# Kernel optimization log

Measured on AMD Instinct MI355X. Metric: run time of the kernel, lower is better.

The kernel has to match this reference:

```python
import jax, jax.numpy as jnp
import numpy as np

B, S, H, NH = 2, 2048, 1024, 16
HD = H // NH  # 64
BASE = 10000.0


def _rope_tables(seq_len, head_dim):
    inv_freq = 1.0 / (BASE ** (jnp.arange(0, head_dim, 2, dtype=jnp.float32) / head_dim))
    t = jnp.arange(seq_len, dtype=jnp.float32)
    freqs = jnp.outer(t, inv_freq)            # [S, HD/2]
    emb = jnp.concatenate([freqs, freqs], -1)  # [S, HD]
    return jnp.cos(emb), jnp.sin(emb)


def _rotate_half(x):
    x1, x2 = jnp.split(x, 2, axis=-1)
    return jnp.concatenate([-x2, x1], axis=-1)


def setup_inputs() -> dict:
    key = jax.random.key(0)
    ks = jax.random.split(key, 5)
    sc = 1.0 / np.sqrt(H)
    return {
        "hidden_states": jax.random.normal(ks[0], (B, S, H), jnp.float32),
        "Wq": jax.random.normal(ks[1], (H, H), jnp.float32) * sc,
        "Wk": jax.random.normal(ks[2], (H, H), jnp.float32) * sc,
        "Wv": jax.random.normal(ks[3], (H, H), jnp.float32) * sc,
        "Wo": jax.random.normal(ks[4], (H, H), jnp.float32) * sc,
    }


def reference(hidden_states, Wq, Wk, Wv, Wo):
    b, s, h = hidden_states.shape
    # nn.Linear: y = x @ W.T
    q = hidden_states @ Wq.T
    k = hidden_states @ Wk.T
    v = hidden_states @ Wv.T
    # [B, NH, S, HD]
    q = q.reshape(b, s, NH, HD).transpose(0, 2, 1, 3)
    k = k.reshape(b, s, NH, HD).transpose(0, 2, 1, 3)
    v = v.reshape(b, s, NH, HD).transpose(0, 2, 1, 3)
    cos, sin = _rope_tables(s, HD)  # [S, HD], broadcast over B, NH
    q = q * cos + _rotate_half(q) * sin
    k = k * cos + _rotate_half(k) * sin
    scores = jnp.einsum('bhqd,bhkd->bhqk', q, k) / jnp.sqrt(jnp.float32(HD))
    probs = jax.nn.softmax(scores, axis=-1)
    ctx = jnp.einsum('bhqk,bhkd->bhqd', probs, v)
    ctx = ctx.transpose(0, 2, 1, 3).reshape(b, s, h)
    return ctx @ Wo.T
```

## Files before the change

### kernel.cpp

```cpp
#include <hip/hip_runtime.h>
#include <hip/hip_bf16.h>
#include <math.h>

typedef __hip_bfloat16 bf16;
typedef float f32x4 __attribute__((ext_vector_type(4)));
typedef float f32x16 __attribute__((ext_vector_type(16)));
typedef short s16x8 __attribute__((ext_vector_type(8)));

#define NB 2
#define SEQ 2048
#define HID 1024
#define NHEAD 16
#define HD 64
#define BH (NB * NHEAD)
#define MROWS (NB * SEQ)
#define QSCL 0.18033688011111793f

static __device__ __forceinline__ f32x4 mfma16(s16x8 a, s16x8 b, f32x4 c) {
  return __builtin_amdgcn_mfma_f32_16x16x32_bf16(a, b, c, 0, 0, 0);
}
static __device__ __forceinline__ f32x16 mfma32(s16x8 a, s16x8 b, f32x16 c) {
  return __builtin_amdgcn_mfma_f32_32x32x16_bf16(a, b, c, 0, 0, 0);
}

static __device__ __forceinline__ void gload_lds16(const bf16* g, bf16* l) {
  __builtin_amdgcn_global_load_lds((const __attribute__((address_space(1))) void*)g,
                                   (__attribute__((address_space(3))) void*)l, 16, 0, 0);
}

static __device__ __forceinline__ unsigned pack_bf16(float a, float b) {
  __hip_bfloat162 t = __float22bfloat162_rn(float2{a, b});
  return *(unsigned*)&t;
}

__global__ __launch_bounds__(256) void prep_kernel(const float* __restrict__ X,
                                                   const float* __restrict__ wq, const float* __restrict__ wk,
                                                   const float* __restrict__ wv, const float* __restrict__ wo,
                                                   bf16* __restrict__ Xb, bf16* __restrict__ wqkv,
                                                   bf16* __restrict__ wob,
                                                   float* __restrict__ ct, float* __restrict__ st) {
  int bid = blockIdx.x, tid = threadIdx.x;
  if (bid < 8192) {
    const float* src;
    bf16* dst;
    int i;
    if (bid < 4096) {
      src = X; dst = Xb;
      i = (bid * 256 + tid) * 4;
    } else {
      int wsel = (bid - 4096) >> 10;
      src = (wsel == 0) ? wq : (wsel == 1) ? wk : (wsel == 2) ? wv : wo;
      dst = (wsel < 3) ? (wqkv + (size_t)wsel * HID * HID) : wob;
      i = (((bid - 4096) & 1023) * 256 + tid) * 4;
    }
    float4 v = *(const float4*)(src + i);
    bf16 a0 = __float2bfloat16(v.x), a1 = __float2bfloat16(v.y);
    bf16 a2 = __float2bfloat16(v.z), a3 = __float2bfloat16(v.w);
    ushort4 u;
    u.x = *(const unsigned short*)&a0;
    u.y = *(const unsigned short*)&a1;
    u.z = *(const unsigned short*)&a2;
    u.w = *(const unsigned short*)&a3;
    *(ushort4*)(dst + i) = u;
  } else {
    int i = (bid - 8192) * 256 + tid;
    int s = i >> 5, j = i & 31;
    float inv = expf(-(float)(2 * j) * (9.210340371976184f / 64.0f));
    float ang = (float)s * inv;
    float sn, cs;
    sincosf(ang, &sn, &cs);
    ct[i] = cs;
    st[i] = sn;
  }
}

template <int MODE>
__global__ __launch_bounds__(256) void gemm_bt(const bf16* __restrict__ A, const bf16* __restrict__ Bm,
                                               float* __restrict__ C,
                                               bf16* __restrict__ Qb, bf16* __restrict__ Kb,
                                               bf16* __restrict__ Vtg,
                                               const float* __restrict__ ct, const float* __restrict__ st,
                                               int M, int N, int K) {
  __shared__ __align__(16) bf16 As[128][32];
  __shared__ __align__(16) bf16 Bs[128][32];
  const int tid = threadIdx.x, lane = tid & 63, wid = tid >> 6;
  const int wm = wid >> 1, wn = wid & 1;
  const int tm = blockIdx.y * 128, tn = blockIdx.x * 128;
  const int lrow = lane >> 2;
  const int lcol = (lane & 3) * 8;

  f32x4 acc[4][4];
#pragma unroll
  for (int i = 0; i < 4; ++i)
#pragma unroll
    for (int j = 0; j < 4; ++j) acc[i][j] = (f32x4){0.f, 0.f, 0.f, 0.f};

  for (int k0 = 0; k0 < K; k0 += 32) {
    __syncthreads();
    {
      int r0 = wid * 32;
      gload_lds16(A  + (size_t)(tm + r0 +      lrow) * K + k0 + lcol, &As[r0][0]);
      gload_lds16(A  + (size_t)(tm + r0 + 16 + lrow) * K + k0 + lcol, &As[r0 + 16][0]);
      gload_lds16(Bm + (size_t)(tn + r0 +      lrow) * K + k0 + lcol, &Bs[r0][0]);
      gload_lds16(Bm + (size_t)(tn + r0 + 16 + lrow) * K + k0 + lcol, &Bs[r0 + 16][0]);
    }
    __syncthreads();
    s16x8 af[4], bfr[4];
#pragma unroll
    for (int mi = 0; mi < 4; ++mi)
      af[mi] = *(const s16x8*)&As[wm * 64 + mi * 16 + (lane & 15)][(lane >> 4) * 8];
#pragma unroll
    for (int ni = 0; ni < 4; ++ni)
      bfr[ni] = *(const s16x8*)&Bs[wn * 64 + ni * 16 + (lane & 15)][(lane >> 4) * 8];
#pragma unroll
    for (int mi = 0; mi < 4; ++mi)
#pragma unroll
      for (int ni = 0; ni < 4; ++ni)
        acc[mi][ni] = mfma16(af[mi], bfr[ni], acc[mi][ni]);
  }

  if (MODE == 0) {
    const int tblk = tn >> 10;
    if (tblk < 2) {
      const float scl = (tblk == 0) ? QSCL : 1.0f;
#pragma unroll
      for (int mi = 0; mi < 4; ++mi) {
#pragma unroll
        for (int r = 0; r < 4; ++r) {
          int row = tm + wm * 64 + mi * 16 + (lane >> 4) * 4 + r;
          int s = row & (SEQ - 1);
#pragma unroll
          for (int p = 0; p < 2; ++p) {
            int j = p * 16 + (lane & 15);
            float c = ct[s * 32 + j], sn = st[s * 32 + j];
            float x0 = acc[mi][p][r], x1 = acc[mi][p + 2][r];
            acc[mi][p][r]     = (x0 * c - x1 * sn) * scl;
            acc[mi][p + 2][r] = (x1 * c + x0 * sn) * scl;
          }
        }
      }
    }
  }

#pragma unroll
  for (int mi = 0; mi < 4; ++mi) {
#pragma unroll
    for (int ni = 0; ni < 4; ++ni) {
#pragma unroll
      for (int r = 0; r < 4; ++r) {
        int row = tm + wm * 64 + mi * 16 + (lane >> 4) * 4 + r;
        int col = tn + wn * 64 + ni * 16 + (lane & 15);
        float v = acc[mi][ni][r];
        if (MODE == 0) {
          int t = col >> 10, c = col & (HID - 1);
          int h = c >> 6, d = c & 63;
          int b = row >> 11, s = row & (SEQ - 1);
          size_t bh = (size_t)(b * NHEAD + h);
          if (t == 0)      Qb[(bh * SEQ + s) * HD + d]  = __float2bfloat16(v);
          else if (t == 1) Kb[(bh * SEQ + s) * HD + d]  = __float2bfloat16(v);
          else             Vtg[(bh * HD + d) * SEQ + s] = __float2bfloat16(v);
        } else {
          C[(size_t)row * N + col] = v;
        }
      }
    }
  }
}

__global__ __launch_bounds__(512, 4) void attn_kernel(const bf16* __restrict__ Q, const bf16* __restrict__ K,
                                                      const bf16* __restrict__ Vt, bf16* __restrict__ ctx) {
  __shared__ __align__(16) bf16 S[32768];
  const int tid = threadIdx.x, l = tid & 63, w = tid >> 6;
  const int lq = l & 31, hi = l >> 5;
  const int grp = w >> 2, wq = w & 3;
  const int gtid = tid & 255;

  const int id = blockIdx.x;
  const int lin = (id & 7) * 64 + (id >> 3);
  const int bh = lin >> 4, qb = lin & 15;

  const bf16* Qp  = Q  + ((size_t)bh * SEQ + qb * 128) * HD;
  const bf16* Kp0 = K  + (size_t)bh * SEQ * HD;
  const bf16* Vp0 = Vt + (size_t)bh * HD * SEQ;

  bf16* Ksg = S + grp * 16384;
  bf16* Vsg = S + grp * 16384 + 8192;

  s16x8 qf[4];
  {
    const bf16* qr = Qp + (wq * 32 + lq) * HD + hi * 8;
#pragma unroll
    for (int ks = 0; ks < 4; ++ks) qf[ks] = *(const s16x8*)(qr + ks * 16);
  }

  s16x8 onesf;
  {
    union { unsigned u[4]; s16x8 v; } oo;
#pragma unroll
    for (int j = 0; j < 4; ++j) oo.u[j] = 0x3F803F80u;
    onesf = oo.v;
  }

  const int s0 = gtid, s1 = gtid + 256;
  const int R0 = s0 >> 3, R1 = s1 >> 3;
  const int c0 = (((s0 & 7) ^ (R0 & 7) ^ ((R0 >> 3) & 3))) * 8;
  const int c1 = (((s1 & 7) ^ (R1 & 7) ^ ((R1 >> 3) & 3))) * 8;
  const int p0 = (R0 & 51) | ((R0 & 4) << 1) | ((R0 & 8) >> 1);
  const int p1 = (R1 & 51) | ((R1 & 4) << 1) | ((R1 & 8) >> 1);
  const bf16* kS0 = Kp0 + p0 * HD + c0;
  const bf16* kS1 = Kp0 + p1 * HD + c1;
  const bf16* vS0 = Vp0 + (size_t)R0 * SEQ + c0;
  const bf16* vS1 = Vp0 + (size_t)R1 * SEQ + c1;

#define STAGE(t, b)                                                        \
  do {                                                                     \
    gload_lds16(kS0 + (size_t)(t) * (64 * HD), Ksg + (b) * 4096 + s0 * 8); \
    gload_lds16(kS1 + (size_t)(t) * (64 * HD), Ksg + (b) * 4096 + s1 * 8); \
    gload_lds16(vS0 + (t) * 64,                Vsg + (b) * 4096 + s0 * 8); \
    gload_lds16(vS1 + (t) * 64,                Vsg + (b) * 4096 + s1 * 8); \
  } while (0)

  const int base = grp * 16;
  STAGE(base + 0, 0);

  f32x16 acc0{}, acc1{};
  f32x16 lones{};

  const int rsx = (lq & 7) ^ ((lq >> 3) & 3);

  const int NSTEP = 16;
  for (int t = 0; t < NSTEP; ++t) {
    const int cur = t & 1;
    __builtin_amdgcn_s_barrier();
    if (t + 1 < NSTEP) {
      STAGE(base + t + 1, cur ^ 1);
      asm volatile("s_waitcnt vmcnt(4)" ::: "memory");
    } else {
      asm volatile("s_waitcnt vmcnt(0)" ::: "memory");
    }
    __builtin_amdgcn_sched_barrier(0);
    __builtin_amdgcn_s_barrier();

    const bf16* Kc = Ksg + cur * 4096;
    const bf16* Vc = Vsg + cur * 4096;

    f32x16 sf0{}, sf1{};
    __builtin_amdgcn_s_setprio(1);
#pragma unroll
    for (int ks = 0; ks < 4; ++ks) {
      const int slot = (ks * 2 + hi) ^ rsx;
      sf0 = mfma32(*(const s16x8*)(Kc + lq * 64 + slot * 8),        qf[ks], sf0);
      sf1 = mfma32(*(const s16x8*)(Kc + (32 + lq) * 64 + slot * 8), qf[ks], sf1);
    }
    __builtin_amdgcn_s_setprio(0);

#pragma unroll
    for (int i = 0; i < 16; ++i) sf0[i] = __builtin_amdgcn_exp2f(sf0[i]);
#pragma unroll
    for (int i = 0; i < 16; ++i) sf1[i] = __builtin_amdgcn_exp2f(sf1[i]);

    s16x8 pf[4];
#pragma unroll
    for (int kt = 0; kt < 4; ++kt) {
      union { unsigned u[4]; s16x8 v; } cc;
#pragma unroll
      for (int vv = 0; vv < 4; ++vv) {
        if (kt < 2) cc.u[vv] = pack_bf16(sf0[(kt & 1) * 8 + 2 * vv], sf0[(kt & 1) * 8 + 2 * vv + 1]);
        else        cc.u[vv] = pack_bf16(sf1[(kt & 1) * 8 + 2 * vv], sf1[(kt & 1) * 8 + 2 * vv + 1]);
      }
      pf[kt] = cc.v;
    }

    __builtin_amdgcn_s_setprio(1);
#pragma unroll
    for (int kt = 0; kt < 4; ++kt) {
      const int slot = (kt * 2 + hi) ^ rsx;
      acc0  = mfma32(pf[kt], *(const s16x8*)(Vc + lq * 64 + slot * 8),        acc0);
      acc1  = mfma32(pf[kt], *(const s16x8*)(Vc + (32 + lq) * 64 + slot * 8), acc1);
      lones = mfma32(pf[kt], onesf, lones);
    }
    __builtin_amdgcn_s_setprio(0);
  }
#undef STAGE

  __syncthreads();

  float* Op = (float*)(S + 16384);
  float* Lp = (float*)S;

  if (grp == 1) {
#pragma unroll
    for (int r = 0; r < 16; ++r) {
      int q = (r & 3) + 8 * (r >> 2) + 4 * hi;
      if (lq == 0) Lp[wq * 32 + q] = lones[r];
      Op[(wq * 32 + q) * 64 + lq]      = acc0[r];
      Op[(wq * 32 + q) * 64 + 32 + lq] = acc1[r];
    }
  }
  __syncthreads();

  if (grp == 0) {
    const int b = bh >> 4, h = bh & (NHEAD - 1);
#pragma unroll
    for (int r = 0; r < 16; ++r) {
      int q = (r & 3) + 8 * (r >> 2) + 4 * hi;
      float inv = 1.0f / (lones[r] + Lp[wq * 32 + q]);
      float o0 = (acc0[r] + Op[(wq * 32 + q) * 64 + lq])      * inv;
      float o1 = (acc1[r] + Op[(wq * 32 + q) * 64 + 32 + lq]) * inv;
      size_t base2 = ((size_t)b * SEQ + qb * 128 + wq * 32 + q) * HID + h * HD + lq;
      ctx[base2]      = __float2bfloat16(o0);
      ctx[base2 + 32] = __float2bfloat16(o1);
    }
  }
}

extern "C" void kernel_launch(void* const* d_in, const int* in_sizes, int n_in,
                              void* d_out, int out_size, void* d_ws, size_t ws_size,
                              hipStream_t stream) {
  const float* X  = (const float*)d_in[0];
  const float* Wq = (const float*)d_in[1];
  const float* Wk = (const float*)d_in[2];
  const float* Wv = (const float*)d_in[3];
  const float* Wo = (const float*)d_in[4];

  char* p = (char*)d_ws;
  bf16* Xb   = (bf16*)p; p += (size_t)MROWS * HID * 2;
  bf16* Wqkv = (bf16*)p; p += (size_t)3 * HID * HID * 2;
  bf16* Wob  = (bf16*)p; p += (size_t)HID * HID * 2;
  bf16* Qb   = (bf16*)p; p += (size_t)BH * SEQ * HD * 2;
  bf16* Kb   = (bf16*)p; p += (size_t)BH * SEQ * HD * 2;
  bf16* Vtg  = (bf16*)p; p += (size_t)BH * HD * SEQ * 2;
  bf16* Cb   = (bf16*)p; p += (size_t)MROWS * HID * 2;
  float* ct  = (float*)p; p += (size_t)SEQ * 32 * 4;
  float* st  = (float*)p; p += (size_t)SEQ * 32 * 4;

  prep_kernel<<<8448, 256, 0, stream>>>(X, Wq, Wk, Wv, Wo, Xb, Wqkv, Wob, ct, st);

  gemm_bt<0><<<dim3(3 * HID / 128, MROWS / 128), 256, 0, stream>>>(
      Xb, Wqkv, nullptr, Qb, Kb, Vtg, ct, st, MROWS, 3 * HID, HID);

  attn_kernel<<<dim3(512), 512, 0, stream>>>(Qb, Kb, Vtg, Cb);

  gemm_bt<1><<<dim3(HID / 128, MROWS / 128), 256, 0, stream>>>(
      Cb, Wob, (float*)d_out, nullptr, nullptr, nullptr, nullptr, nullptr, MROWS, HID, HID);
}
```

Before: 137.8 us.

## Deepen GEMM K-tile to 64 with swizzled LDS and XCD-aware block remap

The projection GEMMs now load a 64-wide K slice per iteration instead of 32, which halves the number of barrier pairs. An XOR swizzle on the LDS column slots avoids bank conflicts on the wider rows. The grid is flattened to 1D and block IDs are remapped so consecutive tiles land on the same XCD, improving L2 reuse of A/B tiles. LDS use doubles to 32KB per block, which may lower occupancy.

```diff
diff --git a/kernel.cpp b/kernel.cpp
--- a/kernel.cpp
+++ b/kernel.cpp
@@ -80,14 +80,15 @@
                                                bf16* __restrict__ Qb, bf16* __restrict__ Kb,
                                                bf16* __restrict__ Vtg,
                                                const float* __restrict__ ct, const float* __restrict__ st,
-                                               int M, int N, int K) {
-  __shared__ __align__(16) bf16 As[128][32];
-  __shared__ __align__(16) bf16 Bs[128][32];
+                                               int M, int N, int K, int NBX) {
+  __shared__ __align__(16) bf16 As[128 * 64];
+  __shared__ __align__(16) bf16 Bs[128 * 64];
   const int tid = threadIdx.x, lane = tid & 63, wid = tid >> 6;
   const int wm = wid >> 1, wn = wid & 1;
-  const int tm = blockIdx.y * 128, tn = blockIdx.x * 128;
-  const int lrow = lane >> 2;
-  const int lcol = (lane & 3) * 8;
+
+  const int cpx = gridDim.x >> 3;
+  const int wg = (blockIdx.x & 7) * cpx + (blockIdx.x >> 3);
+  const int tm = (wg / NBX) * 128, tn = (wg % NBX) * 128;
 
   f32x4 acc[4][4];
 #pragma unroll
@@ -95,28 +96,47 @@
 #pragma unroll
     for (int j = 0; j < 4; ++j) acc[i][j] = (f32x4){0.f, 0.f, 0.f, 0.f};
 
-  for (int k0 = 0; k0 < K; k0 += 32) {
+  const bf16* aS[4];
+  const bf16* bS[4];
+#pragma unroll
+  for (int i = 0; i < 4; ++i) {
+    int seg = tid + 256 * i;
+    int row = seg >> 3, sub = seg & 7;
+    int sc = (sub ^ (row & 7) ^ ((row >> 3) & 3)) * 8;
+    aS[i] = A  + (size_t)(tm + row) * K + sc;
+    bS[i] = Bm + (size_t)(tn + row) * K + sc;
+  }
+
+  for (int k0 = 0; k0 < K; k0 += 64) {
     __syncthreads();
-    {
-      int r0 = wid * 32;
-      gload_lds16(A  + (size_t)(tm + r0 +      lrow) * K + k0 + lcol, &As[r0][0]);
-      gload_lds16(A  + (size_t)(tm + r0 + 16 + lrow) * K + k0 + lcol, &As[r0 + 16][0]);
-      gload_lds16(Bm + (size_t)(tn + r0 +      lrow) * K + k0 + lcol, &Bs[r0][0]);
-      gload_lds16(Bm + (size_t)(tn + r0 + 16 + lrow) * K + k0 + lcol, &Bs[r0 + 16][0]);
+#pragma unroll
+    for (int i = 0; i < 4; ++i) {
+      int seg = tid + 256 * i;
+      gload_lds16(aS[i] + k0, As + seg * 8);
+      gload_lds16(bS[i] + k0, Bs + seg * 8);
     }
     __syncthreads();
-    s16x8 af[4], bfr[4];
-#pragma unroll
-    for (int mi = 0; mi < 4; ++mi)
-      af[mi] = *(const s16x8*)&As[wm * 64 + mi * 16 + (lane & 15)][(lane >> 4) * 8];
-#pragma unroll
-    for (int ni = 0; ni < 4; ++ni)
-      bfr[ni] = *(const s16x8*)&Bs[wn * 64 + ni * 16 + (lane & 15)][(lane >> 4) * 8];
-#pragma unroll
-    for (int mi = 0; mi < 4; ++mi)
-#pragma unroll
-      for (int ni = 0; ni < 4; ++ni)
-        acc[mi][ni] = mfma16(af[mi], bfr[ni], acc[mi][ni]);
+#pragma unroll
+    for (int h = 0; h < 2; ++h) {
+      s16x8 af[4], bfr[4];
+#pragma unroll
+      for (int mi = 0; mi < 4; ++mi) {
+        int row = wm * 64 + mi * 16 + (lane & 15);
+        int slot = (h * 4 + (lane >> 4)) ^ (row & 7) ^ ((row >> 3) & 3);
+        af[mi] = *(const s16x8*)&As[row * 64 + slot * 8];
+      }
+#pragma unroll
+      for (int ni = 0; ni < 4; ++ni) {
+        int row = wn * 64 + ni * 16 + (lane & 15);
+        int slot = (h * 4 + (lane >> 4)) ^ (row & 7) ^ ((row >> 3) & 3);
+        bfr[ni] = *(const s16x8*)&Bs[row * 64 + slot * 8];
+      }
+#pragma unroll
+      for (int mi = 0; mi < 4; ++mi)
+#pragma unroll
+        for (int ni = 0; ni < 4; ++ni)
+          acc[mi][ni] = mfma16(af[mi], bfr[ni], acc[mi][ni]);
+    }
   }
 
   if (MODE == 0) {
@@ -336,11 +356,11 @@
 
   prep_kernel<<<8448, 256, 0, stream>>>(X, Wq, Wk, Wv, Wo, Xb, Wqkv, Wob, ct, st);
 
-  gemm_bt<0><<<dim3(3 * HID / 128, MROWS / 128), 256, 0, stream>>>(
-      Xb, Wqkv, nullptr, Qb, Kb, Vtg, ct, st, MROWS, 3 * HID, HID);
+  gemm_bt<0><<<768, 256, 0, stream>>>(
+      Xb, Wqkv, nullptr, Qb, Kb, Vtg, ct, st, MROWS, 3 * HID, HID, 24);
 
   attn_kernel<<<dim3(512), 512, 0, stream>>>(Qb, Kb, Vtg, Cb);
 
-  gemm_bt<1><<<dim3(HID / 128, MROWS / 128), 256, 0, stream>>>(
-      Cb, Wob, (float*)d_out, nullptr, nullptr, nullptr, nullptr, nullptr, MROWS, HID, HID);
-}
+  gemm_bt<1><<<256, 256, 0, stream>>>(
+      Cb, Wob, (float*)d_out, nullptr, nullptr, nullptr, nullptr, nullptr, MROWS, HID, HID, 8);
+}
```

Measured after the change: 145.4 us. +5.6%, slower.

## Double-buffer GEMM LDS tiles and XOR-swizzle layout to avoid bank conflicts

Applied to the files above, without the earlier changes.

The projection GEMM now keeps two LDS buffers, so the global-to-LDS load of the next K tile is issued before the MFMA work on the current tile, and only one barrier is needed per iteration. The LDS layout is also XOR-swizzled on the 8-element column slot, which is meant to cut bank conflicts on the fragment reads. LDS use doubles. Correctness rests on the single barrier ordering async loads against reads of the buffer being overwritten.

```diff
diff --git a/kernel.cpp b/kernel.cpp
--- a/kernel.cpp
+++ b/kernel.cpp
@@ -81,13 +81,11 @@
                                                bf16* __restrict__ Vtg,
                                                const float* __restrict__ ct, const float* __restrict__ st,
                                                int M, int N, int K) {
-  __shared__ __align__(16) bf16 As[128][32];
-  __shared__ __align__(16) bf16 Bs[128][32];
+  __shared__ __align__(16) bf16 As[2 * 128 * 32];
+  __shared__ __align__(16) bf16 Bs[2 * 128 * 32];
   const int tid = threadIdx.x, lane = tid & 63, wid = tid >> 6;
   const int wm = wid >> 1, wn = wid & 1;
   const int tm = blockIdx.y * 128, tn = blockIdx.x * 128;
-  const int lrow = lane >> 2;
-  const int lcol = (lane & 3) * 8;
 
   f32x4 acc[4][4];
 #pragma unroll
@@ -95,29 +93,54 @@
 #pragma unroll
     for (int j = 0; j < 4; ++j) acc[i][j] = (f32x4){0.f, 0.f, 0.f, 0.f};
 
-  for (int k0 = 0; k0 < K; k0 += 32) {
-    __syncthreads();
-    {
-      int r0 = wid * 32;
-      gload_lds16(A  + (size_t)(tm + r0 +      lrow) * K + k0 + lcol, &As[r0][0]);
-      gload_lds16(A  + (size_t)(tm + r0 + 16 + lrow) * K + k0 + lcol, &As[r0 + 16][0]);
-      gload_lds16(Bm + (size_t)(tn + r0 +      lrow) * K + k0 + lcol, &Bs[r0][0]);
-      gload_lds16(Bm + (size_t)(tn + r0 + 16 + lrow) * K + k0 + lcol, &Bs[r0 + 16][0]);
-    }
-    __syncthreads();
+  const int seg0 = tid, seg1 = tid + 256;
+  const int r0 = seg0 >> 2, sub0 = seg0 & 3;
+  const int r1 = seg1 >> 2, sub1 = seg1 & 3;
+  const int sc0 = (sub0 ^ ((r0 >> 1) & 3)) * 8;
+  const int sc1 = (sub1 ^ ((r1 >> 1) & 3)) * 8;
+  const bf16* aS0 = A  + (size_t)(tm + r0) * K + sc0;
+  const bf16* aS1 = A  + (size_t)(tm + r1) * K + sc1;
+  const bf16* bS0 = Bm + (size_t)(tn + r0) * K + sc0;
+  const bf16* bS1 = Bm + (size_t)(tn + r1) * K + sc1;
+
+#define GSTAGE(k0, b)                                   \
+  do {                                                  \
+    gload_lds16(aS0 + (k0), As + (b) * 4096 + seg0 * 8); \
+    gload_lds16(aS1 + (k0), As + (b) * 4096 + seg1 * 8); \
+    gload_lds16(bS0 + (k0), Bs + (b) * 4096 + seg0 * 8); \
+    gload_lds16(bS1 + (k0), Bs + (b) * 4096 + seg1 * 8); \
+  } while (0)
+
+  const int NT = K >> 5;
+  GSTAGE(0, 0);
+  __syncthreads();
+
+  for (int t = 0; t < NT; ++t) {
+    const int cur = t & 1;
+    if (t + 1 < NT) GSTAGE((t + 1) * 32, cur ^ 1);
+
     s16x8 af[4], bfr[4];
 #pragma unroll
-    for (int mi = 0; mi < 4; ++mi)
-      af[mi] = *(const s16x8*)&As[wm * 64 + mi * 16 + (lane & 15)][(lane >> 4) * 8];
-#pragma unroll
-    for (int ni = 0; ni < 4; ++ni)
-      bfr[ni] = *(const s16x8*)&Bs[wn * 64 + ni * 16 + (lane & 15)][(lane >> 4) * 8];
+    for (int mi = 0; mi < 4; ++mi) {
+      int row = wm * 64 + mi * 16 + (lane & 15);
+      int slot = (lane >> 4) ^ ((row >> 1) & 3);
+      af[mi] = *(const s16x8*)(As + cur * 4096 + row * 32 + slot * 8);
+    }
+#pragma unroll
+    for (int ni = 0; ni < 4; ++ni) {
+      int row = wn * 64 + ni * 16 + (lane & 15);
+      int slot = (lane >> 4) ^ ((row >> 1) & 3);
+      bfr[ni] = *(const s16x8*)(Bs + cur * 4096 + row * 32 + slot * 8);
+    }
 #pragma unroll
     for (int mi = 0; mi < 4; ++mi)
 #pragma unroll
       for (int ni = 0; ni < 4; ++ni)
         acc[mi][ni] = mfma16(af[mi], bfr[ni], acc[mi][ni]);
-  }
+
+    __syncthreads();
+  }
+#undef GSTAGE
 
   if (MODE == 0) {
     const int tblk = tn >> 10;
```

Result: slower. 147.9 us (+7.4%).
